# Performance work log

Measured on AMD Instinct MI355X. Metric: run time of the kernel, lower is better.

The kernel has to match this reference:

```python
import jax, jax.numpy as jnp
import numpy as np

N = 50000          # nodes
E = 1600000        # edges (avg degree 32)
F_IN = 64          # input feature dim
SIZES = (64, 64)   # GATConv output sizes, heads=1
C_OUT = 5          # classifier classes
G = 64             # number of graphs in batch
SLOPE = 0.2        # LeakyReLU negative slope (PyG GATConv default)


def _glorot(key, shape):
    fan_in, fan_out = shape[0], shape[-1]
    s = jnp.sqrt(2.0 / (fan_in + fan_out)).astype(jnp.float32)
    return jax.random.normal(key, shape, jnp.float32) * s


def setup_inputs() -> dict:
    key = jax.random.key(0)
    ks = jax.random.split(key, 16)
    x = jax.random.normal(ks[0], (N, F_IN), jnp.float32)
    edge_index = jax.random.randint(ks[1], (2, E), 0, N)
    batch = jnp.sort(jax.random.randint(ks[2], (N,), 0, G))
    # layer 1 params
    W1 = _glorot(ks[3], (F_IN, SIZES[0]))
    a1s = _glorot(ks[4], (SIZES[0],))
    a1d = _glorot(ks[5], (SIZES[0],))
    b1 = jnp.zeros((SIZES[0],), jnp.float32)
    # layer 2 params
    W2 = _glorot(ks[6], (SIZES[0], SIZES[1]))
    a2s = _glorot(ks[7], (SIZES[1],))
    a2d = _glorot(ks[8], (SIZES[1],))
    b2 = jnp.zeros((SIZES[1],), jnp.float32)
    # final linear
    Wl = _glorot(ks[9], (SIZES[1], C_OUT))
    bl = jnp.zeros((C_OUT,), jnp.float32)
    return {"x": x, "edge_index": edge_index, "batch": batch,
            "W1": W1, "a1s": a1s, "a1d": a1d, "b1": b1,
            "W2": W2, "a2s": a2s, "a2d": a2d, "b2": b2,
            "Wl": Wl, "bl": bl}


def _gat_conv(h_in, W, a_src, a_dst, b, src, dst):
    # PyG GATConv, heads=1: h = W x; e_ij = LeakyReLU(a_src.h_j + a_dst.h_i)
    # alpha = softmax over edges grouped by destination i; out_i = sum alpha*h_j + b
    h = h_in @ W                                   # [N, F]
    e = jax.nn.leaky_relu((h @ a_src)[src] + (h @ a_dst)[dst], SLOPE)  # [E']
    m = jax.ops.segment_max(e, dst, num_segments=N)
    p = jnp.exp(e - m[dst])
    z = jax.ops.segment_sum(p, dst, num_segments=N)
    alpha = p / z[dst]                             # [E']
    out = jax.ops.segment_sum(h[src] * alpha[:, None], dst, num_segments=N)
    return out + b


def reference(x, edge_index, batch, W1, a1s, a1d, b1, W2, a2s, a2d, b2, Wl, bl):
    # add self-loops (PyG GATConv default add_self_loops=True)
    loop = jnp.arange(N, dtype=edge_index.dtype)
    src = jnp.concatenate([edge_index[0], loop])
    dst = jnp.concatenate([edge_index[1], loop])
    h = jax.nn.relu(_gat_conv(x, W1, a1s, a1d, b1, src, dst))
    h = jax.nn.relu(_gat_conv(h, W2, a2s, a2d, b2, src, dst))
    # global max pool per graph
    g = jax.ops.segment_max(h, batch, num_segments=G)   # [G, F]
    # dropout(p=0.3) is identity in eval mode
    return g @ Wl + bl
```

## Files before the change

### kernel.cpp

```cpp
#include <hip/hip_runtime.h>
#include <hip/hip_fp16.h>

#define N_NODES 50000
#define N_EDGES 1600000
#define F 64
#define G_GRAPHS 64
#define C_CLS 5
#define SLOPE 0.2f

#define NBUCKET ((N_NODES + 127) >> 7)
#define ACHUNK 4096
#define NCHUNKS ((N_EDGES + ACHUNK - 1) / ACHUNK)
#define CAP 8192
#define MAXCH 4
#define XPAD 68

__device__ __forceinline__ float lrelu(float x) { return fmaxf(x, SLOPE * x); }


__global__ __launch_bounds__(512) void count_matrix(const int* __restrict__ dst,
                                                    int* __restrict__ Cmat) {
    __shared__ int hist[NBUCKET];
    int tid = threadIdx.x;
    int c = blockIdx.x;
    for (int i = tid; i < NBUCKET; i += 512) hist[i] = 0;
    __syncthreads();
    int base = c * ACHUNK;
    int lim = min(ACHUNK, N_EDGES - base);
    for (int t = tid; t < lim; t += 512) atomicAdd(&hist[dst[base + t] >> 7], 1);
    __syncthreads();
    for (int i = tid; i < NBUCKET; i += 512)
        Cmat[c * NBUCKET + i] = hist[i];
}

__global__ __launch_bounds__(512) void scan_chunk_offsets(const int* __restrict__ Cmat,
                                                          int* __restrict__ Coff,
                                                          int* __restrict__ gcount) {
    __shared__ int sc[512];
    int tid = threadIdx.x;
    int b = blockIdx.x;
    int v = (tid < NCHUNKS) ? Cmat[tid * NBUCKET + b] : 0;
    sc[tid] = v;
    __syncthreads();
    for (int s = 1; s < 512; s <<= 1) {
        int t = (tid >= s) ? sc[tid - s] : 0;
        __syncthreads();
        sc[tid] += t;
        __syncthreads();
    }
    if (tid < NCHUNKS) Coff[b * NCHUNKS + tid] = sc[tid] - v;
    if (tid == 0) gcount[b] = sc[511];
}

__global__ __launch_bounds__(512) void bucket_scatter(
    const int* __restrict__ src, const int* __restrict__ dst,
    const int* __restrict__ Cmat, const int* __restrict__ Coff,
    const int* __restrict__ gcount, unsigned int* __restrict__ bedges) {
    __shared__ int cur[NBUCKET];
    __shared__ int dloc[NBUCKET];
    __shared__ int sc[512];
    __shared__ unsigned long long stage[ACHUNK];
    int tid = threadIdx.x;
    int c = blockIdx.x;
    int base = c * ACHUNK;
    int lim = min(ACHUNK, N_EDGES - base);
    int gb = (tid < NBUCKET) ? gcount[tid] : 0;
    sc[tid] = gb;
    __syncthreads();
    for (int s = 1; s < 512; s <<= 1) {
        int t = (tid >= s) ? sc[tid - s] : 0;
        __syncthreads();
        sc[tid] += t;
        __syncthreads();
    }
    int bbase = sc[tid] - gb;
    __syncthreads();
    int v = (tid < NBUCKET) ? Cmat[c * NBUCKET + tid] : 0;
    sc[tid] = v;
    __syncthreads();
    for (int s = 1; s < 512; s <<= 1) {
        int t = (tid >= s) ? sc[tid - s] : 0;
        __syncthreads();
        sc[tid] += t;
        __syncthreads();
    }
    if (tid < NBUCKET) {
        int loff = sc[tid] - v;
        cur[tid] = loff;
        dloc[tid] = bbase + Coff[tid * NCHUNKS + c] - loff;
    }
    __syncthreads();
    for (int t = tid; t < lim; t += 512) {
        int d = dst[base + t];
        int pos = atomicAdd(&cur[d >> 7], 1);
        stage[pos] = ((unsigned long long)(unsigned)d << 32) | (unsigned)src[base + t];
    }
    __syncthreads();
    for (int t = tid; t < lim; t += 512) {
        unsigned long long p = stage[t];
        int d = (int)(p >> 32);
        bedges[dloc[d >> 7] + t] =
            ((unsigned)(d & 127) << 17) | (unsigned)(p & 0x1ffffull);
    }
}

__global__ __launch_bounds__(512) void bucket_csr(
    const unsigned int* __restrict__ bedges, const int* __restrict__ gcount,
    int* __restrict__ row_ptr, int* __restrict__ csr_src) {
    __shared__ int hist[128];
    __shared__ int sc[128];
    __shared__ int loff[129];
    __shared__ int cur[128];
    __shared__ int scg[512];
    __shared__ int outs[CAP];
    int tid = threadIdx.x;
    int b = blockIdx.x;
    int nbase = b << 7;
    int nlocal = min(128, N_NODES - nbase);
    int gb = (tid < NBUCKET) ? gcount[tid] : 0;
    scg[tid] = gb;
    __syncthreads();
    for (int s = 1; s < 512; s <<= 1) {
        int t = (tid >= s) ? scg[tid - s] : 0;
        __syncthreads();
        scg[tid] += t;
        __syncthreads();
    }
    int cnt = min(gcount[b], CAP);
    int cbase = scg[b] - gcount[b];
    if (tid < 128) { hist[tid] = 0; cur[tid] = 0; }
    __syncthreads();
    for (int t = tid; t < cnt; t += 512)
        atomicAdd(&hist[(int)(bedges[cbase + t] >> 17)], 1);
    __syncthreads();
    if (tid < 128) sc[tid] = hist[tid];
    __syncthreads();
    for (int s = 1; s < 128; s <<= 1) {
        int t = (tid < 128 && tid >= s) ? sc[tid - s] : 0;
        __syncthreads();
        if (tid < 128) sc[tid] += t;
        __syncthreads();
    }
    if (tid < 128) loff[tid + 1] = sc[tid];
    if (tid == 0) loff[0] = 0;
    __syncthreads();
    for (int t = tid; t < cnt; t += 512) {
        unsigned int p = bedges[cbase + t];
        int dl = (int)(p >> 17);
        int r = atomicAdd(&cur[dl], 1);
        outs[loff[dl] + r] = (int)(p & 0x1ffffu);
    }
    __syncthreads();
    for (int t = tid; t < cnt; t += 512) csr_src[cbase + t] = outs[t];
    for (int i = tid; i < nlocal; i += 512) row_ptr[nbase + i] = cbase + loff[i];
    if (b == NBUCKET - 1 && tid == 0) row_ptr[N_NODES] = cbase + loff[nlocal];
}


__global__ __launch_bounds__(256) void gemm_sd_kernel(
    const float* __restrict__ X, const float* __restrict__ W,
    const float* __restrict__ a_s, const float* __restrict__ a_d,
    __half* __restrict__ Hh, float* __restrict__ S, float* __restrict__ D,
    float* __restrict__ gmax0) {
    __shared__ float Wl[F][F];
    __shared__ float Xl[64][XPAD];
    __shared__ float as_l[F], ad_l[F];
    int tid = threadIdx.x;
    if (gmax0 && blockIdx.x == 0) {
        for (int i = tid; i < G_GRAPHS * F; i += 256) gmax0[i] = 0.f;
    }
    for (int i = tid; i < F * F; i += 256) Wl[i >> 6][i & 63] = W[i];
    if (tid < F) { as_l[tid] = a_s[tid]; ad_l[tid] = a_d[tid]; }
    int tile0 = blockIdx.x * 64;
    #pragma unroll
    for (int j = 0; j < 4; j++) {
        int q = tid + (j << 8);
        int row = q >> 4;
        int col = (q & 15) << 2;
        int gr = tile0 + row;
        float4 xv = make_float4(0.f, 0.f, 0.f, 0.f);
        if (gr < N_NODES) xv = *(const float4*)&X[gr * F + col];
        Xl[row][col + 0] = xv.x; Xl[row][col + 1] = xv.y;
        Xl[row][col + 2] = xv.z; Xl[row][col + 3] = xv.w;
    }
    __syncthreads();
    int rsub = tid >> 4;
    int cg = (tid & 15) << 2;
    float acc[4][4];
    #pragma unroll
    for (int i = 0; i < 4; i++)
        #pragma unroll
        for (int c = 0; c < 4; c++) acc[i][c] = 0.f;
    for (int k4 = 0; k4 < F; k4 += 4) {
        float4 w0 = *(const float4*)&Wl[k4 + 0][cg];
        float4 w1 = *(const float4*)&Wl[k4 + 1][cg];
        float4 w2 = *(const float4*)&Wl[k4 + 2][cg];
        float4 w3 = *(const float4*)&Wl[k4 + 3][cg];
        #pragma unroll
        for (int i = 0; i < 4; i++) {
            float4 xv = *(const float4*)&Xl[rsub + (i << 4)][k4];
            acc[i][0] = fmaf(xv.x, w0.x, acc[i][0]); acc[i][1] = fmaf(xv.x, w0.y, acc[i][1]);
            acc[i][2] = fmaf(xv.x, w0.z, acc[i][2]); acc[i][3] = fmaf(xv.x, w0.w, acc[i][3]);
            acc[i][0] = fmaf(xv.y, w1.x, acc[i][0]); acc[i][1] = fmaf(xv.y, w1.y, acc[i][1]);
            acc[i][2] = fmaf(xv.y, w1.z, acc[i][2]); acc[i][3] = fmaf(xv.y, w1.w, acc[i][3]);
            acc[i][0] = fmaf(xv.z, w2.x, acc[i][0]); acc[i][1] = fmaf(xv.z, w2.y, acc[i][1]);
            acc[i][2] = fmaf(xv.z, w2.z, acc[i][2]); acc[i][3] = fmaf(xv.z, w2.w, acc[i][3]);
            acc[i][0] = fmaf(xv.w, w3.x, acc[i][0]); acc[i][1] = fmaf(xv.w, w3.y, acc[i][1]);
            acc[i][2] = fmaf(xv.w, w3.z, acc[i][2]); acc[i][3] = fmaf(xv.w, w3.w, acc[i][3]);
        }
    }
    float as0 = as_l[cg], as1 = as_l[cg + 1], as2 = as_l[cg + 2], as3 = as_l[cg + 3];
    float ad0 = ad_l[cg], ad1 = ad_l[cg + 1], ad2 = ad_l[cg + 2], ad3 = ad_l[cg + 3];
    #pragma unroll
    for (int i = 0; i < 4; i++) {
        int row = tile0 + rsub + (i << 4);
        if (row >= N_NODES) continue;
        __half2 p0 = __floats2half2_rn(acc[i][0], acc[i][1]);
        __half2 p1 = __floats2half2_rn(acc[i][2], acc[i][3]);
        __half2* hp = (__half2*)&Hh[row * F + cg];
        hp[0] = p0; hp[1] = p1;
        float sp = acc[i][0] * as0 + acc[i][1] * as1 + acc[i][2] * as2 + acc[i][3] * as3;
        float dp = acc[i][0] * ad0 + acc[i][1] * ad1 + acc[i][2] * ad2 + acc[i][3] * ad3;
        #pragma unroll
        for (int o = 1; o < 16; o <<= 1) {
            sp += __shfl_xor(sp, o, 64);
            dp += __shfl_xor(dp, o, 64);
        }
        if ((tid & 15) == 0) { S[row] = sp; D[row] = dp; }
    }
}


struct F8 { float v0, v1, v2, v3, v4, v5, v6, v7; };
__device__ __forceinline__ F8 h8_unpack(float4 r) {
    F8 f;
    __half2 a01 = *reinterpret_cast<__half2*>(&r.x);
    __half2 a23 = *reinterpret_cast<__half2*>(&r.y);
    __half2 a45 = *reinterpret_cast<__half2*>(&r.z);
    __half2 a67 = *reinterpret_cast<__half2*>(&r.w);
    f.v0 = __low2float(a01); f.v1 = __high2float(a01);
    f.v2 = __low2float(a23); f.v3 = __high2float(a23);
    f.v4 = __low2float(a45); f.v5 = __high2float(a45);
    f.v6 = __low2float(a67); f.v7 = __high2float(a67);
    return f;
}

#define ACC8(P, G) do { \
    a0 = fmaf(P, (G).v0, a0); a1 = fmaf(P, (G).v1, a1); \
    a2 = fmaf(P, (G).v2, a2); a3 = fmaf(P, (G).v3, a3); \
    a4 = fmaf(P, (G).v4, a4); a5 = fmaf(P, (G).v5, a5); \
    a6 = fmaf(P, (G).v6, a6); a7 = fmaf(P, (G).v7, a7); } while (0)

#define AGG_BODY() \
    int lane = threadIdx.x & 63; \
    int i = (blockIdx.x * blockDim.x + threadIdx.x) >> 6; \
    if (i >= N_NODES) return; \
    int start = row_ptr[i], end = row_ptr[i + 1]; \
    int deg = end - start; \
    int nch = (deg + 63) >> 6; \
    float d_i = Dv[i]; \
    float eself = lrelu(S[i] + d_i); \
    int g  = lane >> 3; \
    int fl = (lane & 7) << 3; \
    float a0 = 0.f, a1 = 0.f, a2 = 0.f, a3 = 0.f; \
    float a4 = 0.f, a5 = 0.f, a6 = 0.f, a7 = 0.f; \
    float z; \
    if (nch <= MAXCH) { \
        int   sj_reg[MAXCH]; \
        float p_reg[MAXCH]; \
        float m = eself; \
        _Pragma("unroll") \
        for (int c = 0; c < MAXCH; c++) { \
            int j = start + (c << 6) + lane; \
            bool v = (c < nch) && (j < end); \
            int sj = v ? csr_src[j] : 0; \
            float e = v ? lrelu(S[sj] + d_i) : -1e30f; \
            sj_reg[c] = sj; \
            p_reg[c] = e; \
            m = fmaxf(m, e); \
        } \
        _Pragma("unroll") \
        for (int o = 32; o > 0; o >>= 1) m = fmaxf(m, __shfl_xor(m, o, 64)); \
        float zlane = 0.f; \
        _Pragma("unroll") \
        for (int c = 0; c < MAXCH; c++) { \
            if (c < nch) { \
                float p = __expf(p_reg[c] - m); \
                p_reg[c] = p; \
                zlane += p; \
            } \
        } \
        _Pragma("unroll") \
        for (int o = 32; o > 0; o >>= 1) zlane += __shfl_xor(zlane, o, 64); \
        float pself = __expf(eself - m); \
        z = zlane + pself; \
        F8 hs = h8_unpack(*(const float4*)&Hh[i * F + fl]); \
        if (g == 0) { \
            a0 = pself * hs.v0; a1 = pself * hs.v1; a2 = pself * hs.v2; a3 = pself * hs.v3; \
            a4 = pself * hs.v4; a5 = pself * hs.v5; a6 = pself * hs.v6; a7 = pself * hs.v7; \
        } \
        _Pragma("unroll") \
        for (int c = 0; c < MAXCH; c++) { \
            if (c >= nch) break; \
            int cnt = min(64, deg - (c << 6)); \
            int iters = (cnt + 7) >> 3; \
            float pj0 = __shfl(p_reg[c], g, 64); \
            int   sj0 = __shfl(sj_reg[c], g, 64); \
            float4 v0 = *(const float4*)&Hh[sj0 * F + fl]; \
            for (int t = 1; t < iters; t++) { \
                int slot = (t << 3) + g; \
                float pj1 = __shfl(p_reg[c], slot, 64); \
                int   sj1 = __shfl(sj_reg[c], slot, 64); \
                float4 v1 = *(const float4*)&Hh[sj1 * F + fl]; \
                F8 gg = h8_unpack(v0); \
                ACC8(pj0, gg); \
                pj0 = pj1; v0 = v1; \
            } \
            F8 gg = h8_unpack(v0); \
            ACC8(pj0, gg); \
        } \
    } else { \
        float m = eself; \
        for (int j = start + lane; j < end; j += 64) \
            m = fmaxf(m, lrelu(S[csr_src[j]] + d_i)); \
        _Pragma("unroll") \
        for (int o = 32; o > 0; o >>= 1) m = fmaxf(m, __shfl_xor(m, o, 64)); \
        float pself = __expf(eself - m); \
        float zlane = 0.f; \
        F8 hs = h8_unpack(*(const float4*)&Hh[i * F + fl]); \
        if (g == 0) { \
            a0 = pself * hs.v0; a1 = pself * hs.v1; a2 = pself * hs.v2; a3 = pself * hs.v3; \
            a4 = pself * hs.v4; a5 = pself * hs.v5; a6 = pself * hs.v6; a7 = pself * hs.v7; \
        } \
        for (int cb = start; cb < end; cb += 64) { \
            int j = cb + lane; \
            bool v = j < end; \
            int sj = v ? csr_src[j] : 0; \
            float p = v ? __expf(lrelu(S[sj] + d_i) - m) : 0.f; \
            zlane += p; \
            int cnt = min(64, end - cb); \
            int iters = (cnt + 7) >> 3; \
            for (int t = 0; t < iters; t++) { \
                int slot = (t << 3) + g; \
                float pj = __shfl(p, slot, 64); \
                int  sjt = __shfl(sj, slot, 64); \
                F8 gg = h8_unpack(*(const float4*)&Hh[sjt * F + fl]); \
                ACC8(pj, gg); \
            } \
        } \
        _Pragma("unroll") \
        for (int o = 32; o > 0; o >>= 1) zlane += __shfl_xor(zlane, o, 64); \
        z = zlane + pself; \
    } \
    _Pragma("unroll") \
    for (int o = 8; o <= 32; o <<= 1) { \
        a0 += __shfl_xor(a0, o, 64); a1 += __shfl_xor(a1, o, 64); \
        a2 += __shfl_xor(a2, o, 64); a3 += __shfl_xor(a3, o, 64); \
        a4 += __shfl_xor(a4, o, 64); a5 += __shfl_xor(a5, o, 64); \
        a6 += __shfl_xor(a6, o, 64); a7 += __shfl_xor(a7, o, 64); \
    } \
    float4 o0, o1; \
    if (g == 0) { \
        float rz = 1.0f / z; \
        float4 b0 = *(const float4*)&bias[fl]; \
        float4 b1 = *(const float4*)&bias[fl + 4]; \
        o0.x = fmaxf(a0 * rz + b0.x, 0.f); \
        o0.y = fmaxf(a1 * rz + b0.y, 0.f); \
        o0.z = fmaxf(a2 * rz + b0.z, 0.f); \
        o0.w = fmaxf(a3 * rz + b0.w, 0.f); \
        o1.x = fmaxf(a4 * rz + b1.x, 0.f); \
        o1.y = fmaxf(a5 * rz + b1.y, 0.f); \
        o1.z = fmaxf(a6 * rz + b1.z, 0.f); \
        o1.w = fmaxf(a7 * rz + b1.w, 0.f); \
    }

__global__ __launch_bounds__(256) void agg_main(
    const __half* __restrict__ Hh, const float* __restrict__ S, const float* __restrict__ Dv,
    const int* __restrict__ row_ptr, const int* __restrict__ csr_src,
    const float* __restrict__ bias, float* __restrict__ OUT) {
    AGG_BODY()
    if (g == 0) {
        *(float4*)&OUT[i * F + fl] = o0;
        *(float4*)&OUT[i * F + fl + 4] = o1;
    }
}

__global__ __launch_bounds__(256) void agg_pool(
    const __half* __restrict__ Hh, const float* __restrict__ S, const float* __restrict__ Dv,
    const int* __restrict__ row_ptr, const int* __restrict__ csr_src,
    const float* __restrict__ bias,
    const int* __restrict__ batch, float* __restrict__ gmax) {
    __shared__ float pout[4][F];
    __shared__ int   pbat[4];
    AGG_BODY()
    int wid = threadIdx.x >> 6;
    if (g == 0) {
        *(float4*)&pout[wid][fl] = o0;
        *(float4*)&pout[wid][fl + 4] = o1;
        if (lane == 0) pbat[wid] = batch[i];
    }
    __syncthreads();
    if (threadIdx.x < F) {
        int f = threadIdx.x;
        int curb = pbat[0];
        float mx = pout[0][f];
        #pragma unroll
        for (int r = 1; r < 4; r++) {
            int b = pbat[r];
            float v = pout[r][f];
            if (b != curb) {
                atomicMax((int*)&gmax[curb * F + f], __float_as_int(mx));
                curb = b; mx = v;
            } else {
                mx = fmaxf(mx, v);
            }
        }
        atomicMax((int*)&gmax[curb * F + f], __float_as_int(mx));
    }
}


__global__ void final_kernel(const float* __restrict__ gmax, const float* __restrict__ Wl,
                             const float* __restrict__ bl, float* __restrict__ out) {
    int g = blockIdx.x;
    int c = threadIdx.x;
    if (c < C_CLS) {
        float acc = bl[c];
        #pragma unroll
        for (int f = 0; f < F; f++) acc = fmaf(gmax[g * F + f], Wl[f * C_CLS + c], acc);
        out[g * C_CLS + c] = acc;
    }
}


extern "C" void kernel_launch(void* const* d_in, const int* in_sizes, int n_in,
                              void* d_out, int out_size, void* d_ws, size_t ws_size,
                              hipStream_t stream) {
    const float* x    = (const float*)d_in[0];
    const int*   ei   = (const int*)d_in[1];
    const int*   batch= (const int*)d_in[2];
    const float* W1   = (const float*)d_in[3];
    const float* a1s  = (const float*)d_in[4];
    const float* a1d  = (const float*)d_in[5];
    const float* b1   = (const float*)d_in[6];
    const float* W2   = (const float*)d_in[7];
    const float* a2s  = (const float*)d_in[8];
    const float* a2d  = (const float*)d_in[9];
    const float* b2   = (const float*)d_in[10];
    const float* Wl   = (const float*)d_in[11];
    const float* bl   = (const float*)d_in[12];
    float* out = (float*)d_out;

    const int* src = ei;
    const int* dst = ei + N_EDGES;

    char* ws = (char*)d_ws;
    size_t off = 0;
    auto alloc = [&](size_t bytes) { size_t o = off; off += (bytes + 255) & ~(size_t)255; return o; };
    int*   row_ptr = (int*)(ws + alloc((size_t)(N_NODES + 1) * 4));
    int*   csr_src = (int*)(ws + alloc((size_t)N_EDGES * 4));
    char*  hAbed   = ws + alloc((size_t)N_NODES * F * 4);
    unsigned int* bedges = (unsigned int*)hAbed;
    __half* Hh     = (__half*)hAbed;
    char*  hBc     = ws + alloc((size_t)N_NODES * F * 4);
    float* hB      = (float*)hBc;
    int*   Cmat    = (int*)hBc;
    int*   Coff    = (int*)(hBc + ((size_t)NCHUNKS * NBUCKET * 4 + 255 & ~(size_t)255));
    float* Sv      = (float*)(ws + alloc((size_t)N_NODES * 4));
    float* Dv      = (float*)(ws + alloc((size_t)N_NODES * 4));
    float* gmax    = (float*)(ws + alloc((size_t)G_GRAPHS * F * 4));
    int*   gcount  = (int*)(ws + alloc((size_t)NBUCKET * 4));

    count_matrix<<<NCHUNKS, 512, 0, stream>>>(dst, Cmat);
    scan_chunk_offsets<<<NBUCKET, 512, 0, stream>>>(Cmat, Coff, gcount);
    bucket_scatter<<<NCHUNKS, 512, 0, stream>>>(src, dst, Cmat, Coff, gcount, bedges);
    bucket_csr<<<NBUCKET, 512, 0, stream>>>(bedges, gcount, row_ptr, csr_src);

    gemm_sd_kernel<<<(N_NODES + 63) / 64, 256, 0, stream>>>(x, W1, a1s, a1d, Hh, Sv, Dv, nullptr);
    agg_main<<<(N_NODES * 64 + 255) / 256, 256, 0, stream>>>(Hh, Sv, Dv, row_ptr, csr_src, b1, hB);

    gemm_sd_kernel<<<(N_NODES + 63) / 64, 256, 0, stream>>>(hB, W2, a2s, a2d, Hh, Sv, Dv, gmax);
    agg_pool<<<(N_NODES * 64 + 255) / 256, 256, 0, stream>>>(Hh, Sv, Dv, row_ptr, csr_src, b2,
                                                             batch, gmax);

    final_kernel<<<G_GRAPHS, 64, 0, stream>>>(gmax, Wl, bl, out);
}
```

Measured before the change: 150.5 us.

## Fuse edge bucket counting with first-layer GEMM in one launch

Merges the edge-histogram count kernel and the layer-1 feature GEMM into a single heterogeneous launch, where the first blocks count and the rest compute H, S and D. This removes one kernel launch and lets the two independent stages overlap on the GPU. The count matrix is transposed to bucket-major so count writes and scan reads become contiguous. Workspace aliasing is replaced with separate buffers, since bedges and Hh are now live at the same time, which raises memory use.

```diff
diff --git a/kernel.cpp b/kernel.cpp
--- a/kernel.cpp
+++ b/kernel.cpp
@@ -11,6 +11,7 @@
 #define NBUCKET ((N_NODES + 127) >> 7)
 #define ACHUNK 4096
 #define NCHUNKS ((N_EDGES + ACHUNK - 1) / ACHUNK)
+#define GTILES ((N_NODES + 63) / 64)
 #define CAP 8192
 #define MAXCH 4
 #define XPAD 68
@@ -18,160 +19,16 @@
 __device__ __forceinline__ float lrelu(float x) { return fmaxf(x, SLOPE * x); }
 
 
-__global__ __launch_bounds__(512) void count_matrix(const int* __restrict__ dst,
-                                                    int* __restrict__ Cmat) {
-    __shared__ int hist[NBUCKET];
-    int tid = threadIdx.x;
-    int c = blockIdx.x;
-    for (int i = tid; i < NBUCKET; i += 512) hist[i] = 0;
-    __syncthreads();
-    int base = c * ACHUNK;
-    int lim = min(ACHUNK, N_EDGES - base);
-    for (int t = tid; t < lim; t += 512) atomicAdd(&hist[dst[base + t] >> 7], 1);
-    __syncthreads();
-    for (int i = tid; i < NBUCKET; i += 512)
-        Cmat[c * NBUCKET + i] = hist[i];
-}
-
-__global__ __launch_bounds__(512) void scan_chunk_offsets(const int* __restrict__ Cmat,
-                                                          int* __restrict__ Coff,
-                                                          int* __restrict__ gcount) {
-    __shared__ int sc[512];
-    int tid = threadIdx.x;
-    int b = blockIdx.x;
-    int v = (tid < NCHUNKS) ? Cmat[tid * NBUCKET + b] : 0;
-    sc[tid] = v;
-    __syncthreads();
-    for (int s = 1; s < 512; s <<= 1) {
-        int t = (tid >= s) ? sc[tid - s] : 0;
-        __syncthreads();
-        sc[tid] += t;
-        __syncthreads();
-    }
-    if (tid < NCHUNKS) Coff[b * NCHUNKS + tid] = sc[tid] - v;
-    if (tid == 0) gcount[b] = sc[511];
-}
-
-__global__ __launch_bounds__(512) void bucket_scatter(
-    const int* __restrict__ src, const int* __restrict__ dst,
-    const int* __restrict__ Cmat, const int* __restrict__ Coff,
-    const int* __restrict__ gcount, unsigned int* __restrict__ bedges) {
-    __shared__ int cur[NBUCKET];
-    __shared__ int dloc[NBUCKET];
-    __shared__ int sc[512];
-    __shared__ unsigned long long stage[ACHUNK];
-    int tid = threadIdx.x;
-    int c = blockIdx.x;
-    int base = c * ACHUNK;
-    int lim = min(ACHUNK, N_EDGES - base);
-    int gb = (tid < NBUCKET) ? gcount[tid] : 0;
-    sc[tid] = gb;
-    __syncthreads();
-    for (int s = 1; s < 512; s <<= 1) {
-        int t = (tid >= s) ? sc[tid - s] : 0;
-        __syncthreads();
-        sc[tid] += t;
-        __syncthreads();
-    }
-    int bbase = sc[tid] - gb;
-    __syncthreads();
-    int v = (tid < NBUCKET) ? Cmat[c * NBUCKET + tid] : 0;
-    sc[tid] = v;
-    __syncthreads();
-    for (int s = 1; s < 512; s <<= 1) {
-        int t = (tid >= s) ? sc[tid - s] : 0;
-        __syncthreads();
-        sc[tid] += t;
-        __syncthreads();
-    }
-    if (tid < NBUCKET) {
-        int loff = sc[tid] - v;
-        cur[tid] = loff;
-        dloc[tid] = bbase + Coff[tid * NCHUNKS + c] - loff;
-    }
-    __syncthreads();
-    for (int t = tid; t < lim; t += 512) {
-        int d = dst[base + t];
-        int pos = atomicAdd(&cur[d >> 7], 1);
-        stage[pos] = ((unsigned long long)(unsigned)d << 32) | (unsigned)src[base + t];
-    }
-    __syncthreads();
-    for (int t = tid; t < lim; t += 512) {
-        unsigned long long p = stage[t];
-        int d = (int)(p >> 32);
-        bedges[dloc[d >> 7] + t] =
-            ((unsigned)(d & 127) << 17) | (unsigned)(p & 0x1ffffull);
-    }
-}
-
-__global__ __launch_bounds__(512) void bucket_csr(
-    const unsigned int* __restrict__ bedges, const int* __restrict__ gcount,
-    int* __restrict__ row_ptr, int* __restrict__ csr_src) {
-    __shared__ int hist[128];
-    __shared__ int sc[128];
-    __shared__ int loff[129];
-    __shared__ int cur[128];
-    __shared__ int scg[512];
-    __shared__ int outs[CAP];
-    int tid = threadIdx.x;
-    int b = blockIdx.x;
-    int nbase = b << 7;
-    int nlocal = min(128, N_NODES - nbase);
-    int gb = (tid < NBUCKET) ? gcount[tid] : 0;
-    scg[tid] = gb;
-    __syncthreads();
-    for (int s = 1; s < 512; s <<= 1) {
-        int t = (tid >= s) ? scg[tid - s] : 0;
-        __syncthreads();
-        scg[tid] += t;
-        __syncthreads();
-    }
-    int cnt = min(gcount[b], CAP);
-    int cbase = scg[b] - gcount[b];
-    if (tid < 128) { hist[tid] = 0; cur[tid] = 0; }
-    __syncthreads();
-    for (int t = tid; t < cnt; t += 512)
-        atomicAdd(&hist[(int)(bedges[cbase + t] >> 17)], 1);
-    __syncthreads();
-    if (tid < 128) sc[tid] = hist[tid];
-    __syncthreads();
-    for (int s = 1; s < 128; s <<= 1) {
-        int t = (tid < 128 && tid >= s) ? sc[tid - s] : 0;
-        __syncthreads();
-        if (tid < 128) sc[tid] += t;
-        __syncthreads();
-    }
-    if (tid < 128) loff[tid + 1] = sc[tid];
-    if (tid == 0) loff[0] = 0;
-    __syncthreads();
-    for (int t = tid; t < cnt; t += 512) {
-        unsigned int p = bedges[cbase + t];
-        int dl = (int)(p >> 17);
-        int r = atomicAdd(&cur[dl], 1);
-        outs[loff[dl] + r] = (int)(p & 0x1ffffu);
-    }
-    __syncthreads();
-    for (int t = tid; t < cnt; t += 512) csr_src[cbase + t] = outs[t];
-    for (int i = tid; i < nlocal; i += 512) row_ptr[nbase + i] = cbase + loff[i];
-    if (b == NBUCKET - 1 && tid == 0) row_ptr[N_NODES] = cbase + loff[nlocal];
-}
-
-
-__global__ __launch_bounds__(256) void gemm_sd_kernel(
+__device__ __forceinline__ void gemm_body(
+    int tile0, int tid,
     const float* __restrict__ X, const float* __restrict__ W,
     const float* __restrict__ a_s, const float* __restrict__ a_d,
-    __half* __restrict__ Hh, float* __restrict__ S, float* __restrict__ D,
-    float* __restrict__ gmax0) {
+    __half* __restrict__ Hh, float* __restrict__ S, float* __restrict__ D) {
     __shared__ float Wl[F][F];
     __shared__ float Xl[64][XPAD];
     __shared__ float as_l[F], ad_l[F];
-    int tid = threadIdx.x;
-    if (gmax0 && blockIdx.x == 0) {
-        for (int i = tid; i < G_GRAPHS * F; i += 256) gmax0[i] = 0.f;
-    }
     for (int i = tid; i < F * F; i += 256) Wl[i >> 6][i & 63] = W[i];
     if (tid < F) { as_l[tid] = a_s[tid]; ad_l[tid] = a_d[tid]; }
-    int tile0 = blockIdx.x * 64;
     #pragma unroll
     for (int j = 0; j < 4; j++) {
         int q = tid + (j << 8);
@@ -231,6 +88,165 @@
 }
 
 
+__global__ __launch_bounds__(256) void count_gemm1(
+    const int* __restrict__ dst, int* __restrict__ Cmat,
+    const float* __restrict__ X, const float* __restrict__ W,
+    const float* __restrict__ a_s, const float* __restrict__ a_d,
+    __half* __restrict__ Hh, float* __restrict__ S, float* __restrict__ D) {
+    int tid = threadIdx.x;
+    if (blockIdx.x < NCHUNKS) {
+        __shared__ int hist[NBUCKET];
+        int c = blockIdx.x;
+        for (int i = tid; i < NBUCKET; i += 256) hist[i] = 0;
+        __syncthreads();
+        int base = c * ACHUNK;
+        int lim = min(ACHUNK, N_EDGES - base);
+        for (int t = tid; t < lim; t += 256) atomicAdd(&hist[dst[base + t] >> 7], 1);
+        __syncthreads();
+        for (int i = tid; i < NBUCKET; i += 256)
+            Cmat[i * NCHUNKS + c] = hist[i];
+    } else {
+        gemm_body((blockIdx.x - NCHUNKS) * 64, tid, X, W, a_s, a_d, Hh, S, D);
+    }
+}
+
+__global__ __launch_bounds__(256) void gemm_sd_kernel(
+    const float* __restrict__ X, const float* __restrict__ W,
+    const float* __restrict__ a_s, const float* __restrict__ a_d,
+    __half* __restrict__ Hh, float* __restrict__ S, float* __restrict__ D,
+    float* __restrict__ gmax0) {
+    int tid = threadIdx.x;
+    if (blockIdx.x == 0) {
+        for (int i = tid; i < G_GRAPHS * F; i += 256) gmax0[i] = 0.f;
+    }
+    gemm_body(blockIdx.x * 64, tid, X, W, a_s, a_d, Hh, S, D);
+}
+
+
+__global__ __launch_bounds__(512) void scan_chunk_offsets(const int* __restrict__ Cmat,
+                                                          int* __restrict__ Coff,
+                                                          int* __restrict__ gcount) {
+    __shared__ int sc[512];
+    int tid = threadIdx.x;
+    int b = blockIdx.x;
+    int v = (tid < NCHUNKS) ? Cmat[b * NCHUNKS + tid] : 0;
+    sc[tid] = v;
+    __syncthreads();
+    for (int s = 1; s < 512; s <<= 1) {
+        int t = (tid >= s) ? sc[tid - s] : 0;
+        __syncthreads();
+        sc[tid] += t;
+        __syncthreads();
+    }
+    if (tid < NCHUNKS) Coff[tid * NBUCKET + b] = sc[tid] - v;
+    if (tid == 0) gcount[b] = sc[511];
+}
+
+__global__ __launch_bounds__(512) void bucket_scatter(
+    const int* __restrict__ src, const int* __restrict__ dst,
+    const int* __restrict__ Cmat, const int* __restrict__ Coff,
+    const int* __restrict__ gcount, unsigned int* __restrict__ bedges) {
+    __shared__ int cur[NBUCKET];
+    __shared__ int dloc[NBUCKET];
+    __shared__ int sc[512];
+    __shared__ unsigned long long stage[ACHUNK];
+    int tid = threadIdx.x;
+    int c = blockIdx.x;
+    int base = c * ACHUNK;
+    int lim = min(ACHUNK, N_EDGES - base);
+    int gb = (tid < NBUCKET) ? gcount[tid] : 0;
+    sc[tid] = gb;
+    __syncthreads();
+    for (int s = 1; s < 512; s <<= 1) {
+        int t = (tid >= s) ? sc[tid - s] : 0;
+        __syncthreads();
+        sc[tid] += t;
+        __syncthreads();
+    }
+    int bbase = sc[tid] - gb;
+    __syncthreads();
+    int v = (tid < NBUCKET) ? Cmat[tid * NCHUNKS + c] : 0;
+    sc[tid] = v;
+    __syncthreads();
+    for (int s = 1; s < 512; s <<= 1) {
+        int t = (tid >= s) ? sc[tid - s] : 0;
+        __syncthreads();
+        sc[tid] += t;
+        __syncthreads();
+    }
+    if (tid < NBUCKET) {
+        int loff = sc[tid] - v;
+        cur[tid] = loff;
+        dloc[tid] = bbase + Coff[c * NBUCKET + tid] - loff;
+    }
+    __syncthreads();
+    for (int t = tid; t < lim; t += 512) {
+        int d = dst[base + t];
+        int pos = atomicAdd(&cur[d >> 7], 1);
+        stage[pos] = ((unsigned long long)(unsigned)d << 32) | (unsigned)src[base + t];
+    }
+    __syncthreads();
+    for (int t = tid; t < lim; t += 512) {
+        unsigned long long p = stage[t];
+        int d = (int)(p >> 32);
+        bedges[dloc[d >> 7] + t] =
+            ((unsigned)(d & 127) << 17) | (unsigned)(p & 0x1ffffull);
+    }
+}
+
+__global__ __launch_bounds__(512) void bucket_csr(
+    const unsigned int* __restrict__ bedges, const int* __restrict__ gcount,
+    int* __restrict__ row_ptr, int* __restrict__ csr_src) {
+    __shared__ int hist[128];
+    __shared__ int sc[128];
+    __shared__ int loff[129];
+    __shared__ int cur[128];
+    __shared__ int scg[512];
+    __shared__ int outs[CAP];
+    int tid = threadIdx.x;
+    int b = blockIdx.x;
+    int nbase = b << 7;
+    int nlocal = min(128, N_NODES - nbase);
+    int gb = (tid < NBUCKET) ? gcount[tid] : 0;
+    scg[tid] = gb;
+    __syncthreads();
+    for (int s = 1; s < 512; s <<= 1) {
+        int t = (tid >= s) ? scg[tid - s] : 0;
+        __syncthreads();
+        scg[tid] += t;
+        __syncthreads();
+    }
+    int cnt = min(gcount[b], CAP);
+    int cbase = scg[b] - gcount[b];
+    if (tid < 128) { hist[tid] = 0; cur[tid] = 0; }
+    __syncthreads();
+    for (int t = tid; t < cnt; t += 512)
+        atomicAdd(&hist[(int)(bedges[cbase + t] >> 17)], 1);
+    __syncthreads();
+    if (tid < 128) sc[tid] = hist[tid];
+    __syncthreads();
+    for (int s = 1; s < 128; s <<= 1) {
+        int t = (tid < 128 && tid >= s) ? sc[tid - s] : 0;
+        __syncthreads();
+        if (tid < 128) sc[tid] += t;
+        __syncthreads();
+    }
+    if (tid < 128) loff[tid + 1] = sc[tid];
+    if (tid == 0) loff[0] = 0;
+    __syncthreads();
+    for (int t = tid; t < cnt; t += 512) {
+        unsigned int p = bedges[cbase + t];
+        int dl = (int)(p >> 17);
+        int r = atomicAdd(&cur[dl], 1);
+        outs[loff[dl] + r] = (int)(p & 0x1ffffu);
+    }
+    __syncthreads();
+    for (int t = tid; t < cnt; t += 512) csr_src[cbase + t] = outs[t];
+    for (int i = tid; i < nlocal; i += 512) row_ptr[nbase + i] = cbase + loff[i];
+    if (b == NBUCKET - 1 && tid == 0) row_ptr[N_NODES] = cbase + loff[nlocal];
+}
+
+
 struct F8 { float v0, v1, v2, v3, v4, v5, v6, v7; };
 __device__ __forceinline__ F8 h8_unpack(float4 r) {
     F8 f;
@@ -459,27 +475,24 @@
     auto alloc = [&](size_t bytes) { size_t o = off; off += (bytes + 255) & ~(size_t)255; return o; };
     int*   row_ptr = (int*)(ws + alloc((size_t)(N_NODES + 1) * 4));
     int*   csr_src = (int*)(ws + alloc((size_t)N_EDGES * 4));
-    char*  hAbed   = ws + alloc((size_t)N_NODES * F * 4);
-    unsigned int* bedges = (unsigned int*)hAbed;
-    __half* Hh     = (__half*)hAbed;
-    char*  hBc     = ws + alloc((size_t)N_NODES * F * 4);
-    float* hB      = (float*)hBc;
-    int*   Cmat    = (int*)hBc;
-    int*   Coff    = (int*)(hBc + ((size_t)NCHUNKS * NBUCKET * 4 + 255 & ~(size_t)255));
+    unsigned int* bedges = (unsigned int*)(ws + alloc((size_t)N_EDGES * 4));
+    __half* Hh     = (__half*)(ws + alloc((size_t)N_NODES * F * 2));
+    float* hB      = (float*)(ws + alloc((size_t)N_NODES * F * 4));
+    int*   Cmat    = (int*)(ws + alloc((size_t)NBUCKET * NCHUNKS * 4));
+    int*   Coff    = (int*)(ws + alloc((size_t)NCHUNKS * NBUCKET * 4));
     float* Sv      = (float*)(ws + alloc((size_t)N_NODES * 4));
     float* Dv      = (float*)(ws + alloc((size_t)N_NODES * 4));
     float* gmax    = (float*)(ws + alloc((size_t)G_GRAPHS * F * 4));
     int*   gcount  = (int*)(ws + alloc((size_t)NBUCKET * 4));
 
-    count_matrix<<<NCHUNKS, 512, 0, stream>>>(dst, Cmat);
+    count_gemm1<<<NCHUNKS + GTILES, 256, 0, stream>>>(dst, Cmat, x, W1, a1s, a1d, Hh, Sv, Dv);
     scan_chunk_offsets<<<NBUCKET, 512, 0, stream>>>(Cmat, Coff, gcount);
     bucket_scatter<<<NCHUNKS, 512, 0, stream>>>(src, dst, Cmat, Coff, gcount, bedges);
     bucket_csr<<<NBUCKET, 512, 0, stream>>>(bedges, gcount, row_ptr, csr_src);
 
-    gemm_sd_kernel<<<(N_NODES + 63) / 64, 256, 0, stream>>>(x, W1, a1s, a1d, Hh, Sv, Dv, nullptr);
     agg_main<<<(N_NODES * 64 + 255) / 256, 256, 0, stream>>>(Hh, Sv, Dv, row_ptr, csr_src, b1, hB);
 
-    gemm_sd_kernel<<<(N_NODES + 63) / 64, 256, 0, stream>>>(hB, W2, a2s, a2d, Hh, Sv, Dv, gmax);
+    gemm_sd_kernel<<<GTILES, 256, 0, stream>>>(hB, W2, a2s, a2d, Hh, Sv, Dv, gmax);
     agg_pool<<<(N_NODES * 64 + 255) / 256, 256, 0, stream>>>(Hh, Sv, Dv, row_ptr, csr_src, b2,
                                                              batch, gmax);
 
```

Result: no change. 149.6 us (median of 3 runs) (-0.6%).
